# Kernel tuning notes

Hardware: AMD Instinct MI355X
Metric: run time of the kernel (lower is better)

The kernel has to match this reference:

```python
import jax, jax.numpy as jnp
import numpy as np

IN_SHAPE = (96, 96)
OUT_SHAPE = (96, 96)
K = 64  # num_components
NUM_IN = 96 * 96
NUM_OUT = 96 * 96


def setup_inputs() -> dict:
    key = jax.random.key(0)
    ks = jax.random.split(key, 5)
    x = jax.random.normal(ks[0], (32,) + IN_SHAPE, dtype=jnp.float32)
    mus = jax.random.uniform(ks[1], (K, 4), dtype=jnp.float32)
    # torch: log_var = ((1/sqrt(K))**2).log() = log(1/K); log_vars = log_var - rand
    log_var0 = jnp.log(jnp.float32(1.0) / jnp.float32(K))
    log_vars = log_var0 - jax.random.uniform(ks[2], (K, 4), dtype=jnp.float32)
    weights = jax.random.uniform(ks[3], (K,), dtype=jnp.float32) - 0.5
    bias = jax.random.uniform(ks[4], (NUM_OUT,), dtype=jnp.float32) - 0.5
    return {"x": x, "mus": mus, "log_vars": log_vars, "weights": weights, "bias": bias}


def _dim_factor(n, mu_k, var_k):
    # exp(-(grid - mu)^2 / (2 var)) per component; shape (n, K)
    grid = jnp.linspace(0.0, 1.0, n).astype(mu_k.dtype)
    return jnp.exp(-((grid[:, None] - mu_k[None, :]) ** 2) / (2.0 * var_k[None, :]))


def reference(x, mus, log_vars, weights, bias):
    vars_ = jnp.exp(log_vars)  # (K, 4)
    # The original sums per-dim log-probs over broadcast (in0,in1,out0,out1,K) then exps;
    # exp of a sum == product of per-dim factors, so we build factor matrices instead.
    in_f = [_dim_factor(IN_SHAPE[i], mus[:, i], vars_[:, i]) for i in range(len(IN_SHAPE))]
    out_f = [_dim_factor(OUT_SHAPE[j], mus[:, len(IN_SHAPE) + j], vars_[:, len(IN_SHAPE) + j])
             for j in range(len(OUT_SHAPE))]
    in_p = jnp.einsum('ak,bk->abk', in_f[0], in_f[1]).reshape(NUM_IN, K)    # (num_in, K)
    out_p = jnp.einsum('ak,bk->abk', out_f[0], out_f[1]).reshape(NUM_OUT, K)  # (num_out, K)
    probs = jnp.einsum('ik,ok,k->io', in_p, out_p, weights)  # (num_in, num_out)
    b = x.shape[0]
    x_out = x.reshape(b, NUM_IN) @ probs + bias
    return x_out.reshape(b, *OUT_SHAPE)
```

## Files before the change

kernel.cpp:

```cpp
#include <hip/hip_runtime.h>
#include <math.h>

#define BATCH   32
#define DIMN    96
#define KCOMP   64
#define NUM_IN  (DIMN*DIMN)
#define NUM_OUT (DIMN*DIMN)


__global__ __launch_bounds__(256) void kA(const float* __restrict__ x,
                                          const float* __restrict__ mus,
                                          const float* __restrict__ log_vars,
                                          float* __restrict__ Yp) {
    __shared__ float f1[DIMN * KCOMP];
    __shared__ float part[4][KCOMP];

    const int tid = threadIdx.x;
    const int bid = blockIdx.x;
    const int b   = bid >> 3;
    const int aq  = bid & 7;

    for (int idx = tid; idx < DIMN * KCOMP; idx += 256) {
        int e = idx >> 6;
        int k = idx & 63;
        float mu = mus[k * 4 + 1];
        float rv = 0.5f * expf(-log_vars[k * 4 + 1]);
        float t  = (float)e * (1.0f / 95.0f) - mu;
        f1[idx] = expf(-(t * t) * rv);
    }
    __syncthreads();

    const int w    = tid >> 6;
    const int lane = tid & 63;
    const int a0   = aq * 12 + w * 3;

    const float* xr = x + b * NUM_IN + a0 * DIMN;

    float acc0 = 0.0f, acc1 = 0.0f, acc2 = 0.0f;
    #pragma unroll 4
    for (int e4 = 0; e4 < DIMN / 4; ++e4) {
        float f10 = f1[(e4 * 4 + 0) * 64 + lane];
        float f11 = f1[(e4 * 4 + 1) * 64 + lane];
        float f12 = f1[(e4 * 4 + 2) * 64 + lane];
        float f13 = f1[(e4 * 4 + 3) * 64 + lane];
        const float4 x0 = *(const float4*)(xr + 0 * DIMN + e4 * 4);
        const float4 x1 = *(const float4*)(xr + 1 * DIMN + e4 * 4);
        const float4 x2 = *(const float4*)(xr + 2 * DIMN + e4 * 4);
        acc0 = fmaf(x0.x, f10, acc0); acc0 = fmaf(x0.y, f11, acc0);
        acc0 = fmaf(x0.z, f12, acc0); acc0 = fmaf(x0.w, f13, acc0);
        acc1 = fmaf(x1.x, f10, acc1); acc1 = fmaf(x1.y, f11, acc1);
        acc1 = fmaf(x1.z, f12, acc1); acc1 = fmaf(x1.w, f13, acc1);
        acc2 = fmaf(x2.x, f10, acc2); acc2 = fmaf(x2.y, f11, acc2);
        acc2 = fmaf(x2.z, f12, acc2); acc2 = fmaf(x2.w, f13, acc2);
    }

    float mu0 = mus[lane * 4 + 0];
    float rv0 = 0.5f * expf(-log_vars[lane * 4 + 0]);
    float g0 = (float)(a0 + 0) * (1.0f / 95.0f) - mu0;
    float g1 = (float)(a0 + 1) * (1.0f / 95.0f) - mu0;
    float g2 = (float)(a0 + 2) * (1.0f / 95.0f) - mu0;
    float yp = expf(-(g0 * g0) * rv0) * acc0
             + expf(-(g1 * g1) * rv0) * acc1
             + expf(-(g2 * g2) * rv0) * acc2;

    part[w][lane] = yp;
    __syncthreads();
    if (tid < KCOMP) {
        float s = part[0][tid] + part[1][tid] + part[2][tid] + part[3][tid];
        Yp[(b * 8 + aq) * KCOMP + tid] = s;
    }
}

__global__ __launch_bounds__(320) void kB(const float* __restrict__ mus,
                                          const float* __restrict__ log_vars,
                                          const float* __restrict__ weights,
                                          const float* __restrict__ bias,
                                          const float* __restrict__ Yp,
                                          float* __restrict__ out) {
    __shared__ float G1[KCOMP * DIMN];
    __shared__ float YG0[KCOMP * 12];
    __shared__ float Yw[KCOMP];
    __shared__ float pacc[2][144][8];

    const int tid = threadIdx.x;
    const int bid = blockIdx.x;
    const int b   = bid >> 3;
    const int oc  = bid & 7;

    if (tid < KCOMP) {
        float s = 0.0f;
        #pragma unroll
        for (int q = 0; q < 8; ++q) s += Yp[(b * 8 + q) * KCOMP + tid];
        Yw[tid] = s * weights[tid];
    }
    for (int idx = tid; idx < KCOMP * DIMN; idx += 320) {
        int k = idx / DIMN;
        int d = idx - k * DIMN;
        float mu = mus[k * 4 + 3];
        float rv = 0.5f * expf(-log_vars[k * 4 + 3]);
        float t  = (float)d * (1.0f / 95.0f) - mu;
        G1[idx] = expf(-(t * t) * rv);
    }
    __syncthreads();

    for (int idx = tid; idx < KCOMP * 12; idx += 320) {
        int k  = idx / 12;
        int cl = idx - k * 12;
        int c  = oc * 12 + cl;
        float mu = mus[k * 4 + 2];
        float rv = 0.5f * expf(-log_vars[k * 4 + 2]);
        float t  = (float)c * (1.0f / 95.0f) - mu;
        YG0[idx] = Yw[k] * expf(-(t * t) * rv);
    }
    __syncthreads();

    if (tid < 288) {
        const int kh = tid / 144;
        const int r  = tid - kh * 144;
        const int p  = r / 24;
        const int dq = r - p * 24;

        float a0 = 0, a1 = 0, a2 = 0, a3 = 0, a4 = 0, a5 = 0, a6 = 0, a7 = 0;
        #pragma unroll 8
        for (int kk = 0; kk < 32; ++kk) {
            int k = kh * 32 + kk;
            const float4 g = *(const float4*)&G1[k * DIMN + dq * 4];
            const float2 y = *(const float2*)&YG0[k * 12 + p * 2];
            a0 = fmaf(y.x, g.x, a0); a1 = fmaf(y.x, g.y, a1);
            a2 = fmaf(y.x, g.z, a2); a3 = fmaf(y.x, g.w, a3);
            a4 = fmaf(y.y, g.x, a4); a5 = fmaf(y.y, g.y, a5);
            a6 = fmaf(y.y, g.z, a6); a7 = fmaf(y.y, g.w, a7);
        }
        float4* pa = (float4*)pacc[kh][r];
        pa[0] = make_float4(a0, a1, a2, a3);
        pa[1] = make_float4(a4, a5, a6, a7);
    }
    __syncthreads();

    if (tid < 144) {
        const int p  = tid / 24;
        const int dq = tid - p * 24;
        const int c0 = oc * 12 + p * 2;
        const int d0 = dq * 4;

        const float4* pa0 = (const float4*)pacc[0][tid];
        const float4* pa1 = (const float4*)pacc[1][tid];

        #pragma unroll
        for (int j = 0; j < 2; ++j) {
            float4 v  = pa0[j];
            float4 w2 = pa1[j];
            int o = (c0 + j) * DIMN + d0;
            float4 bs = *(const float4*)&bias[o];
            float4 res = make_float4(v.x + w2.x + bs.x, v.y + w2.y + bs.y,
                                     v.z + w2.z + bs.z, v.w + w2.w + bs.w);
            *(float4*)&out[b * NUM_OUT + o] = res;
        }
    }
}

extern "C" void kernel_launch(void* const* d_in, const int* in_sizes, int n_in,
                              void* d_out, int out_size, void* d_ws, size_t ws_size,
                              hipStream_t stream) {
    const float* x        = (const float*)d_in[0];
    const float* mus      = (const float*)d_in[1];
    const float* log_vars = (const float*)d_in[2];
    const float* weights  = (const float*)d_in[3];
    const float* bias     = (const float*)d_in[4];
    float* out = (float*)d_out;
    float* Yp  = (float*)d_ws;

    kA<<<256, 256, 0, stream>>>(x, mus, log_vars, Yp);
    kB<<<256, 320, 0, stream>>>(mus, log_vars, weights, bias, Yp, out);
}
```

Baseline: 16.43 us.

## Precompute output Gaussian factors once in kA extra blocks and widen both kernels

```diff
diff --git a/kernel.cpp b/kernel.cpp
--- a/kernel.cpp
+++ b/kernel.cpp
@@ -7,38 +7,66 @@
 #define NUM_IN  (DIMN*DIMN)
 #define NUM_OUT (DIMN*DIMN)
 
+#define YP_OFF 0
+#define F2_OFF 16384
+#define F3_OFF 22528
 
-__global__ __launch_bounds__(256) void kA(const float* __restrict__ x,
+
+__global__ __launch_bounds__(512) void kA(const float* __restrict__ x,
                                           const float* __restrict__ mus,
                                           const float* __restrict__ log_vars,
-                                          float* __restrict__ Yp) {
-    __shared__ float f1[DIMN * KCOMP];
-    __shared__ float part[4][KCOMP];
-
+                                          const float* __restrict__ weights,
+                                          float* __restrict__ ws) {
     const int tid = threadIdx.x;
     const int bid = blockIdx.x;
-    const int b   = bid >> 3;
-    const int aq  = bid & 7;
 
-    for (int idx = tid; idx < DIMN * KCOMP; idx += 256) {
-        int e = idx >> 6;
-        int k = idx & 63;
+    if (bid >= 256) {
+        int idx = (bid - 256) * 512 + tid;
+        int half = idx >= (KCOMP * DIMN);
+        int t = idx - half * (KCOMP * DIMN);
+        int k = t / DIMN;
+        int i = t - k * DIMN;
+        int dim = 2 + half;
+        float mu = mus[k * 4 + dim];
+        float rv = 0.5f * expf(-log_vars[k * 4 + dim]);
+        float g  = (float)i * (1.0f / 95.0f) - mu;
+        float v  = expf(-(g * g) * rv);
+        if (!half) v *= weights[k];
+        ws[(half ? F3_OFF : F2_OFF) + t] = v;
+        return;
+    }
+
+    __shared__ float f1[DIMN * KCOMP];
+    __shared__ float part[8][KCOMP];
+
+    const int b  = bid >> 3;
+    const int aq = bid & 7;
+
+    {
+        const int k  = tid & 63;
+        const int e0 = tid >> 6;
         float mu = mus[k * 4 + 1];
         float rv = 0.5f * expf(-log_vars[k * 4 + 1]);
-        float t  = (float)e * (1.0f / 95.0f) - mu;
-        f1[idx] = expf(-(t * t) * rv);
+        #pragma unroll
+        for (int j = 0; j < 12; ++j) {
+            int e = e0 + j * 8;
+            float t = (float)e * (1.0f / 95.0f) - mu;
+            f1[e * 64 + k] = expf(-(t * t) * rv);
+        }
     }
     __syncthreads();
 
     const int w    = tid >> 6;
     const int lane = tid & 63;
-    const int a0   = aq * 12 + w * 3;
+    const int rg   = w >> 1;
+    const int eh   = w & 1;
+    const int a0   = aq * 12 + rg * 3;
 
     const float* xr = x + b * NUM_IN + a0 * DIMN;
 
     float acc0 = 0.0f, acc1 = 0.0f, acc2 = 0.0f;
     #pragma unroll 4
-    for (int e4 = 0; e4 < DIMN / 4; ++e4) {
+    for (int e4 = eh * 12; e4 < eh * 12 + 12; ++e4) {
         float f10 = f1[(e4 * 4 + 0) * 64 + lane];
         float f11 = f1[(e4 * 4 + 1) * 64 + lane];
         float f12 = f1[(e4 * 4 + 2) * 64 + lane];
@@ -66,64 +94,56 @@
     part[w][lane] = yp;
     __syncthreads();
     if (tid < KCOMP) {
-        float s = part[0][tid] + part[1][tid] + part[2][tid] + part[3][tid];
-        Yp[(b * 8 + aq) * KCOMP + tid] = s;
+        float s = 0.0f;
+        #pragma unroll
+        for (int q = 0; q < 8; ++q) s += part[q][tid];
+        ws[YP_OFF + (b * 8 + aq) * KCOMP + tid] = s;
     }
 }
 
-__global__ __launch_bounds__(320) void kB(const float* __restrict__ mus,
-                                          const float* __restrict__ log_vars,
-                                          const float* __restrict__ weights,
+__global__ __launch_bounds__(576) void kB(const float* __restrict__ ws,
                                           const float* __restrict__ bias,
-                                          const float* __restrict__ Yp,
                                           float* __restrict__ out) {
     __shared__ float G1[KCOMP * DIMN];
     __shared__ float YG0[KCOMP * 12];
-    __shared__ float Yw[KCOMP];
-    __shared__ float pacc[2][144][8];
+    __shared__ float pacc[4 * 144 * 9];
 
     const int tid = threadIdx.x;
     const int bid = blockIdx.x;
     const int b   = bid >> 3;
     const int oc  = bid & 7;
 
-    if (tid < KCOMP) {
-        float s = 0.0f;
+    {
+        const float4* F3g = (const float4*)(ws + F3_OFF);
+        float4* G1v = (float4*)G1;
         #pragma unroll
-        for (int q = 0; q < 8; ++q) s += Yp[(b * 8 + q) * KCOMP + tid];
-        Yw[tid] = s * weights[tid];
+        for (int i = tid; i < (KCOMP * DIMN) / 4; i += 576) G1v[i] = F3g[i];
     }
-    for (int idx = tid; idx < KCOMP * DIMN; idx += 320) {
-        int k = idx / DIMN;
-        int d = idx - k * DIMN;
-        float mu = mus[k * 4 + 3];
-        float rv = 0.5f * expf(-log_vars[k * 4 + 3]);
-        float t  = (float)d * (1.0f / 95.0f) - mu;
-        G1[idx] = expf(-(t * t) * rv);
+    {
+        const float* F2g = ws + F2_OFF;
+        const float* Ypb = ws + YP_OFF + b * 8 * KCOMP;
+        for (int idx = tid; idx < KCOMP * 12; idx += 576) {
+            int k  = idx / 12;
+            int cl = idx - k * 12;
+            float s = 0.0f;
+            #pragma unroll
+            for (int q = 0; q < 8; ++q) s += Ypb[q * KCOMP + k];
+            YG0[idx] = s * F2g[k * DIMN + oc * 12 + cl];
+        }
     }
     __syncthreads();
 
-    for (int idx = tid; idx < KCOMP * 12; idx += 320) {
-        int k  = idx / 12;
-        int cl = idx - k * 12;
-        int c  = oc * 12 + cl;
-        float mu = mus[k * 4 + 2];
-        float rv = 0.5f * expf(-log_vars[k * 4 + 2]);
-        float t  = (float)c * (1.0f / 95.0f) - mu;
-        YG0[idx] = Yw[k] * expf(-(t * t) * rv);
-    }
-    __syncthreads();
-
-    if (tid < 288) {
-        const int kh = tid / 144;
-        const int r  = tid - kh * 144;
+    {
+        const int kq = tid / 144;
+        const int r  = tid - kq * 144;
         const int p  = r / 24;
         const int dq = r - p * 24;
+        const int k0 = kq * 16;
 
         float a0 = 0, a1 = 0, a2 = 0, a3 = 0, a4 = 0, a5 = 0, a6 = 0, a7 = 0;
         #pragma unroll 8
-        for (int kk = 0; kk < 32; ++kk) {
-            int k = kh * 32 + kk;
+        for (int kk = 0; kk < 16; ++kk) {
+            int k = k0 + kk;
             const float4 g = *(const float4*)&G1[k * DIMN + dq * 4];
             const float2 y = *(const float2*)&YG0[k * 12 + p * 2];
             a0 = fmaf(y.x, g.x, a0); a1 = fmaf(y.x, g.y, a1);
@@ -131,9 +151,9 @@
             a4 = fmaf(y.y, g.x, a4); a5 = fmaf(y.y, g.y, a5);
             a6 = fmaf(y.y, g.z, a6); a7 = fmaf(y.y, g.w, a7);
         }
-        float4* pa = (float4*)pacc[kh][r];
-        pa[0] = make_float4(a0, a1, a2, a3);
-        pa[1] = make_float4(a4, a5, a6, a7);
+        float* pa = &pacc[(kq * 144 + r) * 9];
+        pa[0] = a0; pa[1] = a1; pa[2] = a2; pa[3] = a3;
+        pa[4] = a4; pa[5] = a5; pa[6] = a6; pa[7] = a7;
     }
     __syncthreads();
 
@@ -143,18 +163,19 @@
         const int c0 = oc * 12 + p * 2;
         const int d0 = dq * 4;
 
-        const float4* pa0 = (const float4*)pacc[0][tid];
-        const float4* pa1 = (const float4*)pacc[1][tid];
-
+        float s[8];
         #pragma unroll
-        for (int j = 0; j < 2; ++j) {
-            float4 v  = pa0[j];
-            float4 w2 = pa1[j];
-            int o = (c0 + j) * DIMN + d0;
+        for (int j = 0; j < 8; ++j) {
+            s[j] = pacc[(0 * 144 + tid) * 9 + j] + pacc[(1 * 144 + tid) * 9 + j]
+                 + pacc[(2 * 144 + tid) * 9 + j] + pacc[(3 * 144 + tid) * 9 + j];
+        }
+        #pragma unroll
+        for (int jr = 0; jr < 2; ++jr) {
+            int o = (c0 + jr) * DIMN + d0;
             float4 bs = *(const float4*)&bias[o];
-            float4 res = make_float4(v.x + w2.x + bs.x, v.y + w2.y + bs.y,
-                                     v.z + w2.z + bs.z, v.w + w2.w + bs.w);
-            *(float4*)&out[b * NUM_OUT + o] = res;
+            *(float4*)&out[b * NUM_OUT + o] =
+                make_float4(s[jr * 4 + 0] + bs.x, s[jr * 4 + 1] + bs.y,
+                            s[jr * 4 + 2] + bs.z, s[jr * 4 + 3] + bs.w);
         }
     }
 }
@@ -168,8 +189,8 @@
     const float* weights  = (const float*)d_in[3];
     const float* bias     = (const float*)d_in[4];
     float* out = (float*)d_out;
-    float* Yp  = (float*)d_ws;
+    float* ws  = (float*)d_ws;
 
-    kA<<<256, 256, 0, stream>>>(x, mus, log_vars, Yp);
-    kB<<<256, 320, 0, stream>>>(mus, log_vars, weights, bias, Yp, out);
+    kA<<<280, 512, 0, stream>>>(x, mus, log_vars, weights, ws);
+    kB<<<256, 576, 0, stream>>>(ws, bias, out);
 }
```

Result: faster. 14.47 us (-12.0%).
